# Performance work log

Hardware: AMD Instinct MI355X
Metric: run time of the kernel (lower is better)

The kernel has to match this reference:

```python
import jax, jax.numpy as jnp
import numpy as np

B, T, E, H = 2, 2048, 768, 12
DH = E // H  # per-head attention dim
EPS = 1e-5


def setup_inputs() -> dict:
    key = jax.random.key(0)
    ks = jax.random.split(key, 12)
    s = 0.02
    return {
        "x": jax.random.normal(ks[0], (B, T, E), dtype=jnp.float32),
        # stacked per-head projection weights: [H, E, DH], biases [H, DH]
        "Wq": jax.random.normal(ks[1], (H, E, DH), dtype=jnp.float32) * s,
        "bq": jax.random.normal(ks[2], (H, DH), dtype=jnp.float32) * s,
        "Wk": jax.random.normal(ks[3], (H, E, DH), dtype=jnp.float32) * s,
        "bk": jax.random.normal(ks[4], (H, DH), dtype=jnp.float32) * s,
        "Wv": jax.random.normal(ks[5], (H, E, DH), dtype=jnp.float32) * s,
        "bv": jax.random.normal(ks[6], (H, DH), dtype=jnp.float32) * s,
        "Wo": jax.random.normal(ks[7], (E, E), dtype=jnp.float32) * s,
        "bo": jax.random.normal(ks[8], (E,), dtype=jnp.float32) * s,
        "gamma": jnp.ones((E,), dtype=jnp.float32),
        "beta": jnp.zeros((E,), dtype=jnp.float32),
    }


def reference(x, Wq, bq, Wk, bk, Wv, bv, Wo, bo, gamma, beta):
    # per-head projections (heads stacked on axis h)
    q = jnp.einsum("bte,hed->bhtd", x, Wq) + bq[None, :, None, :]
    k = jnp.einsum("bte,hed->bhtd", x, Wk) + bk[None, :, None, :]
    v = jnp.einsum("bte,hed->bhtd", x, Wv) + bv[None, :, None, :]

    scores = jnp.einsum("bhtd,bhsd->bhts", q, k) / jnp.sqrt(jnp.float32(DH))
    causal = jnp.tril(jnp.ones((T, T), dtype=bool))  # True = keep
    scores = jnp.where(causal[None, None], scores, -jnp.inf)
    attn = jax.nn.softmax(scores, axis=-1)
    o = jnp.einsum("bhts,bhsd->bhtd", attn, v)  # [B,H,T,DH]

    # concat heads in head order -> [B,T,E]
    concat = jnp.transpose(o, (0, 2, 1, 3)).reshape(B, T, E)
    proj = concat @ Wo + bo

    # LayerNorm(proj) then residual add
    mu = jnp.mean(proj, axis=-1, keepdims=True)
    var = jnp.mean((proj - mu) ** 2, axis=-1, keepdims=True)
    normed = (proj - mu) * jax.lax.rsqrt(var + EPS) * gamma + beta
    return x + normed
```

## Files before the change

kernel.cpp:

```cpp
#include <hip/hip_runtime.h>
#include <stdint.h>

#define NROWS 4096
#define EMB   768
#define NQKV  2304
#define TSEQ  2048
#define NHEAD 12
#define NBH   24

typedef unsigned short u16;
typedef u16  ushort4v __attribute__((ext_vector_type(4)));
typedef u16  ushort8 __attribute__((ext_vector_type(8)));
typedef __bf16 bf16x8 __attribute__((ext_vector_type(8)));
typedef float f32x4 __attribute__((ext_vector_type(4)));

typedef const __attribute__((address_space(1))) void* gas_ptr;
typedef __attribute__((address_space(3))) void* las_ptr;

__device__ __forceinline__ u16 f2bf(float f) {
  union { float f; uint32_t u; } v; v.f = f;
  uint32_t u = v.u;
  return (u16)((u + 0x7fffu + ((u >> 16) & 1u)) >> 16);
}
__device__ __forceinline__ uint32_t cvtpk(float lo, float hi) {
  uint32_t r;
  asm("v_cvt_pk_bf16_f32 %0, %1, %2" : "=v"(r) : "v"(lo), "v"(hi));
  return r;
}

#define VMCNT0 asm volatile("s_waitcnt vmcnt(0)" ::: "memory")
#define LGKM0  asm volatile("s_waitcnt lgkmcnt(0)" ::: "memory")
#define SBAR   __builtin_amdgcn_s_barrier()
#define SCHED0 __builtin_amdgcn_sched_barrier(0)

__global__ void k_zero(uint32_t* cnt) {
  if (threadIdx.x < 8) cnt[threadIdx.x] = 0;
}

__global__ __launch_bounds__(256) void k_pack_x(const float* __restrict__ x, u16* __restrict__ xb) {
  int i = (blockIdx.x * 256 + threadIdx.x) * 8;
  float4 a = *(const float4*)(x + i);
  float4 b = *(const float4*)(x + i + 4);
  uint4 o;
  o.x = cvtpk(a.x, a.y); o.y = cvtpk(a.z, a.w);
  o.z = cvtpk(b.x, b.y); o.w = cvtpk(b.z, b.w);
  *(uint4*)(xb + i) = o;
}

__global__ __launch_bounds__(256) void k_pack_wqkv(const float* __restrict__ Wq, const float* __restrict__ Wk,
                            const float* __restrict__ Wv, const float* __restrict__ bq,
                            const float* __restrict__ bk, const float* __restrict__ bv,
                            u16* __restrict__ wt, float* __restrict__ bias) {
  int idx = blockIdx.x * 256 + threadIdx.x;
  if (idx >= NQKV * EMB) return;
  int n = idx / EMB, e = idx - n * EMB;
  int sel = n / EMB;
  int c = n - sel * EMB;
  int h = c >> 6, d = c & 63;
  const float* W = sel == 0 ? Wq : (sel == 1 ? Wk : Wv);
  wt[idx] = f2bf(W[((size_t)h * EMB + e) * 64 + d]);
  if (e == 0) {
    const float* bs = sel == 0 ? bq : (sel == 1 ? bk : bv);
    bias[n] = bs[h * 64 + d];
  }
}

__global__ __launch_bounds__(256) void k_pack_wo(const float* __restrict__ Wo, u16* __restrict__ wot) {
  int idx = blockIdx.x * 256 + threadIdx.x;
  if (idx >= EMB * EMB) return;
  int n = idx / EMB, e = idx - n * EMB;
  wot[idx] = f2bf(Wo[(size_t)e * EMB + n]);
}

template<int BM, int BN, int OUT_MODE>
__global__ __launch_bounds__(256) void k_gemm(const u16* __restrict__ A, const u16* __restrict__ Bt,
                                              const float* __restrict__ bias, void* __restrict__ Cout,
                                              u16* __restrict__ vtout, int M, int N, int K) {
  constexpr int MR = BM / 32, NR = BN / 32;
  __shared__ u16 lds_a[BM * 64];
  __shared__ u16 lds_b[BN * 64];
  int tid = threadIdx.x;
  int w = tid >> 6, lane = tid & 63;
  int wr = w >> 1, wc = w & 1;
  int m0 = blockIdx.x * BM, n0 = blockIdx.y * BN;
  int lrow = lane & 15, g = lane >> 4;

  f32x4 zero = {0.f, 0.f, 0.f, 0.f};
  f32x4 acc[MR][NR];
  for (int m = 0; m < MR; ++m) for (int n = 0; n < NR; ++n) acc[m][n] = zero;

  int l8 = lane >> 3, c8 = lane & 7;

  for (int k0 = 0; k0 < K; k0 += 64) {
#pragma unroll
    for (int i = 0; i < BM / 32; ++i) {
      int row = w * (BM / 4) + 8 * i + l8;
      int c16 = c8 ^ (row & 7);
      const u16* ga = A + (size_t)(m0 + row) * K + k0 + c16 * 8;
      __builtin_amdgcn_global_load_lds((gas_ptr)ga, (las_ptr)(lds_a + (w * (BM / 4) + 8 * i) * 64), 16, 0, 0);
    }
#pragma unroll
    for (int i = 0; i < BN / 32; ++i) {
      int row = w * (BN / 4) + 8 * i + l8;
      int c16 = c8 ^ (row & 7);
      const u16* gb = Bt + (size_t)(n0 + row) * K + k0 + c16 * 8;
      __builtin_amdgcn_global_load_lds((gas_ptr)gb, (las_ptr)(lds_b + (w * (BN / 4) + 8 * i) * 64), 16, 0, 0);
    }
    __syncthreads();
    bf16x8 af[MR][2], bfr[NR][2];
#pragma unroll
    for (int m = 0; m < MR; ++m)
#pragma unroll
      for (int kc = 0; kc < 2; ++kc) {
        int row = wr * (BM / 2) + m * 16 + lrow;
        int ch = (kc * 4 + g) ^ (row & 7);
        af[m][kc] = *(const bf16x8*)(lds_a + row * 64 + ch * 8);
      }
#pragma unroll
    for (int n = 0; n < NR; ++n)
#pragma unroll
      for (int kc = 0; kc < 2; ++kc) {
        int row = wc * (BN / 2) + n * 16 + lrow;
        int ch = (kc * 4 + g) ^ (row & 7);
        bfr[n][kc] = *(const bf16x8*)(lds_b + row * 64 + ch * 8);
      }
#pragma unroll
    for (int kc = 0; kc < 2; ++kc)
#pragma unroll
      for (int m = 0; m < MR; ++m)
#pragma unroll
        for (int n = 0; n < NR; ++n)
          acc[m][n] = __builtin_amdgcn_mfma_f32_16x16x32_bf16(af[m][kc], bfr[n][kc], acc[m][n], 0, 0, 0);
    __syncthreads();
  }

#pragma unroll
  for (int m = 0; m < MR; ++m)
#pragma unroll
    for (int n = 0; n < NR; ++n) {
      int col = n0 + wc * (BN / 2) + n * 16 + lrow;
      float bcol = bias[col];
      int row0 = m0 + wr * (BM / 2) + m * 16 + 4 * g;
      if (OUT_MODE == 2 && col >= 2 * EMB) {
        int c = col - 2 * EMB;
        int hh = c >> 6, d = c & 63;
        int bb = row0 >> 11, t = row0 & 2047;
        int y = bb * NHEAD + hh;
        ushort4v pk;
#pragma unroll
        for (int r = 0; r < 4; ++r) pk[r] = f2bf(acc[m][n][r] + bcol);
        *(ushort4v*)(vtout + (size_t)(y * 64 + d) * TSEQ + t) = pk;
      } else {
#pragma unroll
        for (int r = 0; r < 4; ++r) {
          int row = row0 + r;
          float v = acc[m][n][r] + bcol;
          if (OUT_MODE == 1) ((float*)Cout)[(size_t)row * N + col] = v;
          else               ((u16*)Cout)[(size_t)row * N + col] = f2bf(v);
        }
      }
    }
}

__global__ __launch_bounds__(256, 4) void k_attn(const u16* __restrict__ qkv, const u16* __restrict__ vt,
                                                 u16* __restrict__ aout, uint32_t* __restrict__ cnt) {
  __shared__ u16 kbuf[2][64 * 64];
  __shared__ u16 vbuf[2][64 * 64];
  __shared__ u16 pbuf[4][16 * 64];
  __shared__ int task_s;
  int tid = threadIdx.x;
  int w = tid >> 6, lane = tid & 63;
  int ql = lane & 15, g = lane >> 4;
  int xcd = blockIdx.x & 7;
  const float sc2 = 0.18033688f;
  u16* pw = &pbuf[w][0];
  int swz = (ql & 7) << 3;
  int l8 = lane >> 3, c8 = lane & 7;

  for (;;) {
    if (tid == 0) task_s = (int)atomicAdd(&cnt[xcd], 1u);
    __syncthreads();
    int tau = task_s;
    __syncthreads();
    if (tau >= 96) break;

    int idx = tau / 3;
    int yl = tau - idx * 3;
    int qb = 31 - idx;
    int y = xcd * 3 + yl;
    int b = y / NHEAD, h = y - b * NHEAD;
    int nt = qb + 1;
    int qrow0w = qb * 64 + w * 16;
    int qg = qrow0w + ql;

    const u16* qp = qkv + (size_t)(b * TSEQ + qg) * NQKV + h * 64;
    bf16x8 bq0 = *(const bf16x8*)(qp + g * 8);
    bf16x8 bq1 = *(const bf16x8*)(qp + 32 + g * 8);

    const u16* kst = qkv + (size_t)(b * TSEQ) * NQKV + EMB + h * 64;
    const u16* vst = vt + (size_t)y * 64 * TSEQ;

    f32x4 zero = {0.f, 0.f, 0.f, 0.f};
    f32x4 o[4]; for (int n = 0; n < 4; ++n) o[n] = zero;
    float lr = 0.f;

    auto STAGE = [&](int bi, int t_) {
#pragma unroll
      for (int i = 0; i < 2; ++i) {
        int row = i * 32 + 8 * w + l8;
        int c16 = c8 ^ (row & 7);
        const u16* gk = kst + (size_t)(t_ * 64 + row) * NQKV + c16 * 8;
        __builtin_amdgcn_global_load_lds((gas_ptr)gk, (las_ptr)(&kbuf[bi][(i * 32 + 8 * w) * 64]), 16, 0, 0);
        const u16* gv = vst + (size_t)row * TSEQ + t_ * 64 + c16 * 8;
        __builtin_amdgcn_global_load_lds((gas_ptr)gv, (las_ptr)(&vbuf[bi][(i * 32 + 8 * w) * 64]), 16, 0, 0);
      }
    };

    STAGE(0, 0);
    for (int t = 0; t < nt; ++t) {
      int cur = t & 1;
      VMCNT0;
      SBAR;
      if (t + 1 < nt) STAGE(cur ^ 1, t + 1);

      const u16* kb = &kbuf[cur][0];
      const u16* vb = &vbuf[cur][0];
      int s0 = t * 64;

      f32x4 st[4];
#pragma unroll
      for (int sblk = 0; sblk < 4; ++sblk) {
        int row = sblk * 16 + ql;
        bf16x8 ka0 = *(const bf16x8*)(kb + ((row * 64 + 8 * g) ^ swz));
        bf16x8 ka1 = *(const bf16x8*)(kb + ((row * 64 + 32 + 8 * g) ^ swz));
        f32x4 acc = zero;
        acc = __builtin_amdgcn_mfma_f32_16x16x32_bf16(ka0, bq0, acc, 0, 0, 0);
        acc = __builtin_amdgcn_mfma_f32_16x16x32_bf16(ka1, bq1, acc, 0, 0, 0);
        st[sblk] = acc;
      }

      bool lastt = (t == nt - 1);
      float e[4][4];
#pragma unroll
      for (int sblk = 0; sblk < 4; ++sblk)
#pragma unroll
        for (int r = 0; r < 4; ++r) {
          float vv = __builtin_fmaf(st[sblk][r], sc2, -2.0f);
          if (lastt) {
            int sg = s0 + sblk * 16 + 4 * g + r;
            if (sg > qg) vv = -1e30f;
          }
          float ee = __builtin_amdgcn_exp2f(vv);
          e[sblk][r] = ee;
          lr += ee;
        }

#pragma unroll
      for (int sblk = 0; sblk < 4; ++sblk) {
        uint2 dw;
        dw.x = cvtpk(e[sblk][0], e[sblk][1]);
        dw.y = cvtpk(e[sblk][2], e[sblk][3]);
        *(uint2*)(pw + ((ql * 64 + sblk * 16 + 4 * g) ^ swz)) = dw;
      }
      LGKM0; SCHED0;
      bf16x8 ap0 = *(const bf16x8*)(pw + ((ql * 64 + 8 * g) ^ swz));
      bf16x8 ap1 = *(const bf16x8*)(pw + ((ql * 64 + 32 + 8 * g) ^ swz));

#pragma unroll
      for (int n = 0; n < 4; ++n) {
        int row = n * 16 + ql;
        bf16x8 vb0 = *(const bf16x8*)(vb + ((row * 64 + 8 * g) ^ swz));
        bf16x8 vb1 = *(const bf16x8*)(vb + ((row * 64 + 32 + 8 * g) ^ swz));
        o[n] = __builtin_amdgcn_mfma_f32_16x16x32_bf16(ap0, vb0, o[n], 0, 0, 0);
        o[n] = __builtin_amdgcn_mfma_f32_16x16x32_bf16(ap1, vb1, o[n], 0, 0, 0);
      }
    }

    float lw = lr;
    lw += __shfl_xor(lw, 16);
    lw += __shfl_xor(lw, 32);
    float linv = 1.0f / lw;
    float li[4];
#pragma unroll
    for (int r = 0; r < 4; ++r) li[r] = __shfl(linv, 4 * g + r);
#pragma unroll
    for (int n = 0; n < 4; ++n)
#pragma unroll
      for (int r = 0; r < 4; ++r) {
        int q = qrow0w + 4 * g + r;
        aout[(size_t)(b * TSEQ + q) * EMB + h * 64 + n * 16 + ql] = f2bf(o[n][r] * li[r]);
      }
  }
}

__global__ __launch_bounds__(256) void k_ln_res(const float* __restrict__ proj, const float* __restrict__ x,
                                                const float* __restrict__ gamma, const float* __restrict__ beta,
                                                float* __restrict__ out) {
  __shared__ float smem[2][4];
  int row = blockIdx.x;
  const float* pr = proj + (size_t)row * EMB;
  const float* xr = x + (size_t)row * EMB;
  float* orow = out + (size_t)row * EMB;
  int tid = threadIdx.x;
  float v[3];
  float s = 0.f, s2 = 0.f;
#pragma unroll
  for (int i = 0; i < 3; ++i) { v[i] = pr[tid + 256 * i]; s += v[i]; s2 += v[i] * v[i]; }
#pragma unroll
  for (int m = 1; m < 64; m <<= 1) { s += __shfl_xor(s, m); s2 += __shfl_xor(s2, m); }
  int w = tid >> 6, lane = tid & 63;
  if (lane == 0) { smem[0][w] = s; smem[1][w] = s2; }
  __syncthreads();
  s  = smem[0][0] + smem[0][1] + smem[0][2] + smem[0][3];
  s2 = smem[1][0] + smem[1][1] + smem[1][2] + smem[1][3];
  float mu = s * (1.f / EMB);
  float var = s2 * (1.f / EMB) - mu * mu;
  float rstd = rsqrtf(var + 1e-5f);
#pragma unroll
  for (int i = 0; i < 3; ++i) {
    int c = tid + 256 * i;
    orow[c] = xr[c] + (v[i] - mu) * rstd * gamma[c] + beta[c];
  }
}

extern "C" void kernel_launch(void* const* d_in, const int* in_sizes, int n_in,
                              void* d_out, int out_size, void* d_ws, size_t ws_size,
                              hipStream_t stream) {
  const float* x     = (const float*)d_in[0];
  const float* Wq    = (const float*)d_in[1];
  const float* bq    = (const float*)d_in[2];
  const float* Wk    = (const float*)d_in[3];
  const float* bk    = (const float*)d_in[4];
  const float* Wv    = (const float*)d_in[5];
  const float* bv    = (const float*)d_in[6];
  const float* Wo    = (const float*)d_in[7];
  const float* bo    = (const float*)d_in[8];
  const float* gamma = (const float*)d_in[9];
  const float* beta  = (const float*)d_in[10];
  float* out = (float*)d_out;

  char* ws = (char*)d_ws;
  size_t off = 0;
  u16* xb    = (u16*)(ws + off); off += (size_t)NROWS * EMB * 2;
  u16* wqkvt = (u16*)(ws + off); off += (size_t)NQKV * EMB * 2;
  u16* wot   = (u16*)(ws + off); off += (size_t)EMB * EMB * 2;
  float* bqkv = (float*)(ws + off); off += (size_t)NQKV * 4;
  uint32_t* cnt = (uint32_t*)(ws + off); off += 64;
  u16* qkv   = (u16*)(ws + off); off += (size_t)NROWS * NQKV * 2;
  u16* vt    = (u16*)(ws + off); off += (size_t)NBH * 64 * TSEQ * 2;
  u16* aout  = (u16*)(ws + off); off += (size_t)NROWS * EMB * 2;
  float* proj = (float*)qkv;

  k_zero<<<1, 64, 0, stream>>>(cnt);
  k_pack_x<<<NROWS * EMB / (256 * 8), 256, 0, stream>>>(x, xb);
  k_pack_wqkv<<<(NQKV * EMB + 255) / 256, 256, 0, stream>>>(Wq, Wk, Wv, bq, bk, bv, wqkvt, bqkv);
  k_pack_wo<<<(EMB * EMB + 255) / 256, 256, 0, stream>>>(Wo, wot);
  k_gemm<128, 128, 2><<<dim3(NROWS / 128, NQKV / 128), 256, 0, stream>>>(xb, wqkvt, bqkv, qkv, vt, NROWS, NQKV, EMB);
  k_attn<<<dim3(1024), 256, 0, stream>>>(qkv, vt, aout, cnt);
  k_gemm<128, 64, 1><<<dim3(NROWS / 128, EMB / 64), 256, 0, stream>>>(aout, wot, bo, proj, nullptr, NROWS, EMB, EMB);
  k_ln_res<<<NROWS, 256, 0, stream>>>(proj, x, gamma, beta, out);
}
```

Baseline: 134.9 us.

## Split long causal attention query blocks across two KV ranges and combine partials

Query blocks 16-31 are split into two tasks, one covering KV tiles 0-15 and one covering the rest. Each writes unnormalized bf16 partial outputs and row sums to workspace, and a new combine kernel sums them and normalizes. Because the softmax uses a fixed max offset, the partials can be added directly. The aim is to shorten the longest tasks and balance work across the persistent workgroups. The cost is an extra kernel launch, extra partial-output traffic, and a second bf16 rounding of the partials.

```diff
diff --git a/kernel.cpp b/kernel.cpp
--- a/kernel.cpp
+++ b/kernel.cpp
@@ -21,6 +21,10 @@
   union { float f; uint32_t u; } v; v.f = f;
   uint32_t u = v.u;
   return (u16)((u + 0x7fffu + ((u >> 16) & 1u)) >> 16);
+}
+__device__ __forceinline__ float bf2f(u16 u) {
+  union { uint32_t u; float f; } v; v.u = ((uint32_t)u) << 16;
+  return v.f;
 }
 __device__ __forceinline__ uint32_t cvtpk(float lo, float hi) {
   uint32_t r;
@@ -163,7 +167,8 @@
 }
 
 __global__ __launch_bounds__(256, 4) void k_attn(const u16* __restrict__ qkv, const u16* __restrict__ vt,
-                                                 u16* __restrict__ aout, uint32_t* __restrict__ cnt) {
+                                                 u16* __restrict__ aout, uint32_t* __restrict__ cnt,
+                                                 u16* __restrict__ pO, float* __restrict__ pL) {
   __shared__ u16 kbuf[2][64 * 64];
   __shared__ u16 vbuf[2][64 * 64];
   __shared__ u16 pbuf[4][16 * 64];
@@ -182,14 +187,16 @@
     __syncthreads();
     int tau = task_s;
     __syncthreads();
-    if (tau >= 96) break;
-
-    int idx = tau / 3;
-    int yl = tau - idx * 3;
-    int qb = 31 - idx;
+    if (tau >= 144) break;
+
+    int rank = tau / 3, yl = tau - rank * 3;
+    int qb, t0, t1ex, cslot; bool direct;
+    if (rank < 16)       { qb = 16 + rank; t0 = 0;  t1ex = 16;     cslot = 0; direct = false; }
+    else if (!(rank & 1)){ int i = (rank - 16) >> 1; qb = 31 - i; t0 = 16; t1ex = qb + 1; cslot = 1; direct = false; }
+    else                 { int i = (rank - 16) >> 1; qb = 15 - i; t0 = 0;  t1ex = qb + 1; cslot = 0; direct = true; }
+
     int y = xcd * 3 + yl;
     int b = y / NHEAD, h = y - b * NHEAD;
-    int nt = qb + 1;
     int qrow0w = qb * 64 + w * 16;
     int qg = qrow0w + ql;
 
@@ -216,12 +223,12 @@
       }
     };
 
-    STAGE(0, 0);
-    for (int t = 0; t < nt; ++t) {
+    STAGE(t0 & 1, t0);
+    for (int t = t0; t < t1ex; ++t) {
       int cur = t & 1;
       VMCNT0;
       SBAR;
-      if (t + 1 < nt) STAGE(cur ^ 1, t + 1);
+      if (t + 1 < t1ex) STAGE(cur ^ 1, t + 1);
 
       const u16* kb = &kbuf[cur][0];
       const u16* vb = &vbuf[cur][0];
@@ -239,7 +246,7 @@
         st[sblk] = acc;
       }
 
-      bool lastt = (t == nt - 1);
+      bool lastt = (t == qb);
       float e[4][4];
 #pragma unroll
       for (int sblk = 0; sblk < 4; ++sblk)
@@ -279,18 +286,61 @@
     float lw = lr;
     lw += __shfl_xor(lw, 16);
     lw += __shfl_xor(lw, 32);
-    float linv = 1.0f / lw;
-    float li[4];
-#pragma unroll
-    for (int r = 0; r < 4; ++r) li[r] = __shfl(linv, 4 * g + r);
-#pragma unroll
-    for (int n = 0; n < 4; ++n)
-#pragma unroll
-      for (int r = 0; r < 4; ++r) {
-        int q = qrow0w + 4 * g + r;
-        aout[(size_t)(b * TSEQ + q) * EMB + h * 64 + n * 16 + ql] = f2bf(o[n][r] * li[r]);
-      }
+
+    if (direct) {
+      float linv = 1.0f / lw;
+      float li[4];
+#pragma unroll
+      for (int r = 0; r < 4; ++r) li[r] = __shfl(linv, 4 * g + r);
+#pragma unroll
+      for (int n = 0; n < 4; ++n)
+#pragma unroll
+        for (int r = 0; r < 4; ++r) {
+          int q = qrow0w + 4 * g + r;
+          aout[(size_t)(b * TSEQ + q) * EMB + h * 64 + n * 16 + ql] = f2bf(o[n][r] * li[r]);
+        }
+    } else {
+      int blk = y * 16 + (qb - 16);
+      u16* po = pO + ((size_t)blk * 2 + cslot) * 4096;
+      float* pl = pL + ((size_t)blk * 2 + cslot) * 64;
+      if (g == 0) pl[w * 16 + ql] = lw;
+#pragma unroll
+      for (int n = 0; n < 4; ++n)
+#pragma unroll
+        for (int r = 0; r < 4; ++r) {
+          int qloc = w * 16 + 4 * g + r;
+          po[qloc * 64 + n * 16 + ql] = f2bf(o[n][r]);
+        }
+    }
   }
+}
+
+__global__ __launch_bounds__(256) void k_combine(const u16* __restrict__ pO, const float* __restrict__ pL,
+                                                 u16* __restrict__ aout) {
+  int blk = blockIdx.x;
+  int y = blk >> 4, qb = 16 + (blk & 15);
+  int b = y / NHEAD, h = y - b * NHEAD;
+  int tid = threadIdx.x;
+  int row = tid >> 2, c0 = (tid & 3) * 16;
+  const u16* p0 = pO + ((size_t)blk * 2) * 4096 + row * 64 + c0;
+  const u16* p1 = p0 + 4096;
+  float l = pL[blk * 128 + row] + pL[blk * 128 + 64 + row];
+  float rinv = 1.0f / l;
+  ushort8 a0 = *(const ushort8*)(p0);
+  ushort8 a1 = *(const ushort8*)(p0 + 8);
+  ushort8 b0 = *(const ushort8*)(p1);
+  ushort8 b1 = *(const ushort8*)(p1 + 8);
+  ushort8 o0, o1;
+#pragma unroll
+  for (int j = 0; j < 8; j += 2) {
+    uint32_t w0 = cvtpk((bf2f(a0[j]) + bf2f(b0[j])) * rinv, (bf2f(a0[j+1]) + bf2f(b0[j+1])) * rinv);
+    o0[j] = (u16)(w0 & 0xffff); o0[j+1] = (u16)(w0 >> 16);
+    uint32_t w1 = cvtpk((bf2f(a1[j]) + bf2f(b1[j])) * rinv, (bf2f(a1[j+1]) + bf2f(b1[j+1])) * rinv);
+    o1[j] = (u16)(w1 & 0xffff); o1[j+1] = (u16)(w1 >> 16);
+  }
+  u16* dst = aout + (size_t)(b * TSEQ + qb * 64 + row) * EMB + h * 64 + c0;
+  *(ushort8*)dst = o0;
+  *(ushort8*)(dst + 8) = o1;
 }
 
 __global__ __launch_bounds__(256) void k_ln_res(const float* __restrict__ proj, const float* __restrict__ x,
@@ -349,6 +399,8 @@
   u16* qkv   = (u16*)(ws + off); off += (size_t)NROWS * NQKV * 2;
   u16* vt    = (u16*)(ws + off); off += (size_t)NBH * 64 * TSEQ * 2;
   u16* aout  = (u16*)(ws + off); off += (size_t)NROWS * EMB * 2;
+  u16* pO    = (u16*)(ws + off); off += (size_t)NBH * 16 * 2 * 4096 * 2;
+  float* pL  = (float*)(ws + off); off += (size_t)NBH * 16 * 2 * 64 * 4;
   float* proj = (float*)qkv;
 
   k_zero<<<1, 64, 0, stream>>>(cnt);
@@ -356,7 +408,8 @@
   k_pack_wqkv<<<(NQKV * EMB + 255) / 256, 256, 0, stream>>>(Wq, Wk, Wv, bq, bk, bv, wqkvt, bqkv);
   k_pack_wo<<<(EMB * EMB + 255) / 256, 256, 0, stream>>>(Wo, wot);
   k_gemm<128, 128, 2><<<dim3(NROWS / 128, NQKV / 128), 256, 0, stream>>>(xb, wqkvt, bqkv, qkv, vt, NROWS, NQKV, EMB);
-  k_attn<<<dim3(1024), 256, 0, stream>>>(qkv, vt, aout, cnt);
+  k_attn<<<dim3(1024), 256, 0, stream>>>(qkv, vt, aout, cnt, pO, pL);
+  k_combine<<<dim3(NBH * 16), 256, 0, stream>>>(pO, pL, aout);
   k_gemm<128, 64, 1><<<dim3(NROWS / 128, EMB / 64), 256, 0, stream>>>(aout, wot, bo, proj, nullptr, NROWS, EMB, EMB);
   k_ln_res<<<NROWS, 256, 0, stream>>>(proj, x, gamma, beta, out);
 }
```

After: 137.1 us. Within noise of the previous version (+1.6%).
